# Kernel optimization log

Measured on AMD Instinct MI355X. Metric: run time of the kernel, lower is better.

The kernel has to match this reference:

```python
import jax, jax.numpy as jnp
import numpy as np
from jax import lax

N = 10000
T_CTX = 24
HORIZON = 40
T = T_CTX + HORIZON  # 64
N_ENV = 17
COORD = 2
N_IN = N_ENV + COORD + 2  # 21
H = 128


def _lstm_cell(inp, h, c, Wih, Whh, bih, bhh):
    # torch.nn.LSTMCell gate order: input, forget, cell, output
    g = inp @ Wih.T + bih + h @ Whh.T + bhh  # [N, 4H]
    i, f, gg, o = jnp.split(g, 4, axis=1)
    c2 = jax.nn.sigmoid(f) * c + jax.nn.sigmoid(i) * jnp.tanh(gg)
    h2 = jax.nn.sigmoid(o) * jnp.tanh(c2)
    return h2, c2


def setup_inputs() -> dict:
    key = jax.random.key(0)
    ks = jax.random.split(key, 30)
    kaiming = lambda k, shp: jax.random.normal(k, shp, jnp.float32) * np.sqrt(2.0 / shp[-1]).astype(np.float32)
    u = 1.0 / np.sqrt(H).astype(np.float32)
    uni = lambda k, shp: jax.random.uniform(k, shp, jnp.float32, -u, u)
    inp = {
        'x': jax.random.uniform(ks[0], (N, T), jnp.float32),
        'coords': jax.random.normal(ks[1], (N, COORD), jnp.float32),
        'env': jax.random.normal(ks[2], (N, N_ENV, T), jnp.float32),
        'areas': jax.random.uniform(ks[3], (N,), jnp.float32),
        # encoder params (2 stacked H->H LSTM layers)
        'W_enc_in': kaiming(ks[4], (H, N_IN)),
        'enc_Wih': uni(ks[5], (2, 4 * H, H)),
        'enc_Whh': uni(ks[6], (2, 4 * H, H)),
        'enc_bih': uni(ks[7], (2, 4 * H)),
        'enc_bhh': uni(ks[8], (2, 4 * H)),
        # decoder NodeLSTM params
        'W_dec_in': kaiming(ks[9], (H, N_IN)),
        'in_Wih': uni(ks[10], (4 * H, 2 * H)),  # lstm_in takes [proj, enc_state]
        'in_Whh': uni(ks[11], (4 * H, H)),
        'in_bih': uni(ks[12], (4 * H,)),
        'in_bhh': uni(ks[13], (4 * H,)),
        'd_Wih': uni(ks[14], (4 * H, H)),
        'd_Whh': uni(ks[15], (4 * H, H)),
        'd_bih': uni(ks[16], (4 * H,)),
        'd_bhh': uni(ks[17], (4 * H,)),
        # SourceSinkMLP params
        'mlp_W1': kaiming(ks[18], (H, H + N_IN)),
        'mlp_b1': jnp.zeros((H,), jnp.float32),
        'mlp_W2': kaiming(ks[19], (2, H)),
        'mlp_b2': jnp.zeros((2,), jnp.float32),
    }
    return inp


def reference(x, coords, env, areas, W_enc_in, enc_Wih, enc_Whh, enc_bih, enc_bhh,
              W_dec_in, in_Wih, in_Whh, in_bih, in_bhh, d_Wih, d_Whh, d_bih, d_bhh,
              mlp_W1, mlp_b1, mlp_W2, mlp_b2):
    n = x.shape[0]
    areas_c = areas[:, None]
    x_seq = x.T                              # [T, N]
    env_seq = jnp.transpose(env, (2, 0, 1))  # [T, N, N_ENV]
    z = jnp.zeros((n, H), x.dtype)

    # ---- RecurrentEncoder over context steps ----
    def enc_step(carry, xs):
        h0, c0, h1, c1 = carry
        xt, et = xs
        inp = jnp.concatenate([xt[:, None], coords, et, areas_c], axis=1)  # [N, N_IN]
        proj = inp @ W_enc_in.T
        h0, c0 = _lstm_cell(proj, h0, c0, enc_Wih[0], enc_Whh[0], enc_bih[0], enc_bhh[0])
        h1, c1 = _lstm_cell(h0, h1, c1, enc_Wih[1], enc_Whh[1], enc_bih[1], enc_bhh[1])
        return (h0, c0, h1, c1), None

    (h0, c0, h1, c1), _ = lax.scan(enc_step, (z, z, z, z), (x_seq[:T_CTX], env_seq[:T_CTX]))
    enc_state = h1  # captured once in setup_states, constant over the forecast

    # ---- NodeLSTM + SourceSinkMLP rollout over the horizon ----
    def dec_step(carry, et):
        xc, h0, c0, h1, c1 = carry  # xc: [N, 1]
        inp = jnp.concatenate([xc, coords, et, areas_c], axis=1)  # [N, N_IN]
        proj = jnp.concatenate([inp @ W_dec_in.T, enc_state], axis=1)  # [N, 2H]
        h0, c0 = _lstm_cell(proj, h0, c0, in_Wih, in_Whh, in_bih, in_bhh)
        h1, c1 = _lstm_cell(h0, h1, c1, d_Wih, d_Whh, d_bih, d_bhh)
        # SourceSinkMLP
        zmid = jax.nn.leaky_relu(jnp.concatenate([h1, inp], axis=1) @ mlp_W1.T + mlp_b1)
        ss = zmid @ mlp_W2.T + mlp_b2  # [N, 2]
        source = jax.nn.sigmoid(ss[:, :1])
        sink = jax.nn.sigmoid(ss[:, 1:2]) * xc
        xn = xc + source - sink
        return (xn, h0, c0, h1, c1), xn[:, 0]

    x0 = x[:, T_CTX - 1][:, None]
    _, ys = lax.scan(dec_step, (x0, h0, c0, h1, c1), env_seq[T_CTX:T_CTX + HORIZON])
    return ys.T  # [N, HORIZON]
```

## Files before the change

kernel.cpp:

```cpp
#include <hip/hip_runtime.h>

#define NTOT  10000
#define TALL  64
#define TCTX  24
#define HOR   40
#define HH    128
#define G4    512
#define NENV  17
#define SAMP  16

typedef __attribute__((ext_vector_type(8))) short  bf16x8;
typedef __attribute__((ext_vector_type(4))) float  f32x4;
typedef unsigned short u16;

#define SEG_W0E   0
#define SEG_W0D   8192
#define SEG_WIH1  16384
#define SEG_WHH1  24576
#define SEG_DWIH  32768
#define SEG_DWHH  40960
#define SEG_M0E   49152
#define SEG_MDE   51200
#define SEG_WIHH  53248
#define SEG_W1H   61440
#define SEG_W1I   63488
#define NFRAGS    64000

#define L_MDL   0
#define L_W1H   32768
#define L_W1I   65536
#define L_BASE  73728
#define L_H0    106496
#define L_H1    115200
#define L_ZMS   123904
#define L_INPS  128256
#define L_XBLK  129536
#define L_W2L   131072
#define L_XCS   132096
#define SMEM_TOTAL 132160

__device__ __forceinline__ float sigf(float v)   { return 1.0f/(1.0f + __expf(-v)); }
__device__ __forceinline__ float tanhf_(float v) { return 1.0f - 2.0f/(__expf(2.0f*v) + 1.0f); }
__device__ __forceinline__ u16 f2bf(float f){
    unsigned int u = __float_as_uint(f);
    u += 0x7fffu + ((u >> 16) & 1u);
    return (u16)(u >> 16);
}
__device__ __forceinline__ float bf2f(u16 h){ return __uint_as_float(((unsigned int)h) << 16); }

__global__ void fold_kernel(const float* __restrict__ enc_Wih, const float* __restrict__ enc_Whh,
                            const float* __restrict__ W_enc_in,
                            const float* __restrict__ in_Wih,  const float* __restrict__ in_Whh,
                            const float* __restrict__ W_dec_in,
                            const float* __restrict__ dWih,    const float* __restrict__ dWhh,
                            const float* __restrict__ mlp_W1,  const float* __restrict__ mlp_b1,
                            const float* __restrict__ enc_bih, const float* __restrict__ enc_bhh,
                            const float* __restrict__ in_bih,  const float* __restrict__ in_bhh,
                            void* __restrict__ ws)
{
    int fid = blockIdx.x*256 + threadIdx.x;
    if (fid >= NFRAGS) return;
    const int lane = fid & 63;
    const int cc = lane & 15;
    const int kg = lane >> 4;
    float vals[8];

    if (fid < 49152) {
        int segi = fid >> 13;
        int loc  = fid & 8191;
        int gt   = loc >> 8;
        int kb   = (loc >> 6) & 3;
        int r    = gt*16 + cc;
        int k0   = kb*32 + kg*8;
        const float* src;
        switch (segi) {
            case 0: src = enc_Whh;          break;
            case 1: src = in_Whh;           break;
            case 2: src = enc_Wih + 65536;  break;
            case 3: src = enc_Whh + 65536;  break;
            case 4: src = dWih;             break;
            default: src = dWhh;            break;
        }
        #pragma unroll
        for (int j = 0; j < 8; ++j) vals[j] = src[(size_t)r*128 + k0 + j];
    } else if (fid < 53248) {
        int loc = fid - 49152;
        int which = loc >> 11; loc &= 2047;
        int gt = loc >> 6;
        int r  = gt*16 + cc;
        int k0 = kg*8;
        const float* A = which ? (in_Wih + (size_t)r*256) : (enc_Wih + (size_t)r*128);
        const float* B = which ? W_dec_in : W_enc_in;
        float bias = which ? (in_bih[r] + in_bhh[r]) : (enc_bih[r] + enc_bhh[r]);
        #pragma unroll
        for (int j = 0; j < 8; ++j) {
            int k = k0 + j;
            float v = 0.f;
            int c = (k <= 16) ? (3 + k) : (k == 17 ? 0 : (k == 18 ? 1 : (k == 19 ? 2 : (k == 20 ? 20 : -1))));
            if (k == 21) v = bias;
            else if (c >= 0) {
                float a = 0.f;
                for (int h = 0; h < HH; ++h) a = fmaf(A[h], B[h*21 + c], a);
                v = a;
            }
            vals[j] = v;
        }
    } else if (fid < 61440) {
        int loc = fid - 53248;
        int gt = loc >> 8; int kb = (loc >> 6) & 3;
        int r = gt*16 + cc; int k0 = kb*32 + kg*8;
        #pragma unroll
        for (int j = 0; j < 8; ++j) vals[j] = in_Wih[(size_t)r*256 + 128 + k0 + j];
    } else if (fid < 63488) {
        int loc = fid - 61440;
        int gt = loc >> 8; int kb = (loc >> 6) & 3;
        int r = gt*16 + cc; int k0 = kb*32 + kg*8;
        #pragma unroll
        for (int j = 0; j < 8; ++j) vals[j] = mlp_W1[(size_t)r*149 + k0 + j];
    } else {
        int loc = fid - 63488;
        int gt = loc >> 6;
        int r = gt*16 + cc; int k0 = kg*8;
        #pragma unroll
        for (int j = 0; j < 8; ++j) {
            int k = k0 + j; float v = 0.f;
            if (k <= 16)      v = mlp_W1[(size_t)r*149 + 131 + k];
            else if (k == 17) v = mlp_W1[(size_t)r*149 + 128];
            else if (k == 18) v = mlp_W1[(size_t)r*149 + 129];
            else if (k == 19) v = mlp_W1[(size_t)r*149 + 130];
            else if (k == 20) v = mlp_W1[(size_t)r*149 + 148];
            else if (k == 21) v = mlp_b1[r];
            vals[j] = v;
        }
    }
    union { uint4 u4; u16 us[8]; } pk;
    #pragma unroll
    for (int j = 0; j < 8; ++j) pk.us[j] = f2bf(vals[j]);
    *(uint4*)((char*)ws + (size_t)fid*16) = pk.u4;
}

__global__ __launch_bounds__(512, 1)
void lstm_main(const float* __restrict__ x, const float* __restrict__ coords,
               const float* __restrict__ env, const float* __restrict__ areas,
               const float* __restrict__ enc_bih, const float* __restrict__ enc_bhh,
               const float* __restrict__ dbih,   const float* __restrict__ dbhh,
               const float* __restrict__ mlp_W2, const float* __restrict__ mlp_b2,
               const void* __restrict__ ws, float* __restrict__ out)
{
    extern __shared__ char smem[];
    u16*   MdL  = (u16*)(smem + L_MDL);
    u16*   W1Hl = (u16*)(smem + L_W1H);
    u16*   W1Il = (u16*)(smem + L_W1I);
    float* baseL= (float*)(smem + L_BASE);
    u16*   zms  = (u16*)(smem + L_ZMS);
    u16*   inps = (u16*)(smem + L_INPS);
    float* xblk = (float*)(smem + L_XBLK);
    float* w2l  = (float*)(smem + L_W2L);
    float* xcs  = (float*)(smem + L_XCS);

    const int tid  = threadIdx.x;
    const int lane = tid & 63;
    const int wid  = tid >> 6;
    const int cc   = lane & 15;
    const int kg   = lane >> 4;
    const int s0   = blockIdx.x * SAMP;
    const char* wsb = (const char*)ws;
    const f32x4 zero4 = {0.f, 0.f, 0.f, 0.f};

    #pragma unroll
    for (int i = 0; i < 4; ++i) {
        ((uint4*)(smem + L_MDL))[i*512 + tid] = ((const uint4*)wsb)[SEG_M0E + i*512 + tid];
        ((uint4*)(smem + L_W1H))[i*512 + tid] = ((const uint4*)wsb)[SEG_W1H + i*512 + tid];
    }
    ((uint4*)(smem + L_W1I))[tid] = ((const uint4*)wsb)[SEG_W1I + tid];
    for (int i = tid; i < 2176; i += 512) {
        ((u16*)(smem + L_H0 + 4352))[i] = 0;
        ((u16*)(smem + L_H1 + 4352))[i] = 0;
    }
    if (tid < 384) xblk[tid] = x[(size_t)(s0 + tid/24)*TALL + (tid % 24)];
    if (tid < 256) w2l[tid] = mlp_W2[tid];
    if (tid < SAMP) {
        inps[tid*40 + 18] = f2bf(coords[(size_t)(s0+tid)*2 + 0]);
        inps[tid*40 + 19] = f2bf(coords[(size_t)(s0+tid)*2 + 1]);
        inps[tid*40 + 20] = f2bf(areas[s0+tid]);
        inps[tid*40 + 21] = 0x3F80;
        #pragma unroll
        for (int c = 22; c < 32; ++c) inps[tid*40 + c] = 0;
    }

    const int sA = tid / NENV, eA = tid - sA*NENV;
    const bool envth = (tid < 272);
    const float* envp = env + ((size_t)(s0 + (envth ? sA : 0))*NENV + (envth ? eA : 0))*TALL;
    float evA = envth ? envp[0] : 0.f;

    bf16x8 W0r[16], WrA[16], WrB[16];
    float  lb1[4];
    #pragma unroll
    for (int g = 0; g < 4; ++g) {
        int gt = g*8 + wid;
        #pragma unroll
        for (int kb = 0; kb < 4; ++kb) {
            W0r[g*4+kb] = *(const bf16x8*)(wsb + ((size_t)(SEG_W0E  + (gt*4+kb)*64 + lane))*16);
            WrA[g*4+kb] = *(const bf16x8*)(wsb + ((size_t)(SEG_WIH1 + (gt*4+kb)*64 + lane))*16);
            WrB[g*4+kb] = *(const bf16x8*)(wsb + ((size_t)(SEG_WHH1 + (gt*4+kb)*64 + lane))*16);
        }
        int grow = gt*16 + cc;
        lb1[g] = enc_bih[512 + grow] + enc_bhh[512 + grow];
    }

    float c0r[4] = {0.f,0.f,0.f,0.f};
    float c1r[4] = {0.f,0.f,0.f,0.f};
    __syncthreads();

    #pragma unroll 1
    for (int t = 0; t < TCTX; ++t) {
        u16* h0w = (u16*)(smem + L_H0 + (t&1)*4352);
        u16* h0r = (u16*)(smem + L_H0 + ((t&1)^1)*4352);
        u16* h1w = (u16*)(smem + L_H1 + (t&1)*4352);
        u16* h1r = (u16*)(smem + L_H1 + ((t&1)^1)*4352);

        if (envth)    inps[sA*40 + eA]  = f2bf(evA);
        if (tid < 16) inps[tid*40 + 17] = f2bf(xblk[tid*24 + t]);
        __syncthreads();
        if (envth && t+1 < TALL) evA = envp[t+1];

        bf16x8 ia = *(const bf16x8*)(inps + cc*40 + kg*8);
        f32x4 acc[4];
        #pragma unroll
        for (int g = 0; g < 4; ++g) {
            bf16x8 md = *(const bf16x8*)(MdL + ((size_t)((g*8+wid)*64 + lane))*8);
            acc[g] = __builtin_amdgcn_mfma_f32_16x16x32_bf16(ia, md, zero4, 0, 0, 0);
        }
        #pragma unroll
        for (int kb = 0; kb < 4; ++kb) {
            bf16x8 ha = *(const bf16x8*)(h0r + cc*136 + kb*32 + kg*8);
            #pragma unroll
            for (int g = 0; g < 4; ++g)
                acc[g] = __builtin_amdgcn_mfma_f32_16x16x32_bf16(ha, W0r[g*4+kb], acc[g], 0, 0, 0);
        }
        float h2[4];
        #pragma unroll
        for (int r = 0; r < 4; ++r) {
            float c2 = fmaf(sigf(acc[1][r]), c0r[r], sigf(acc[0][r])*tanhf_(acc[2][r]));
            c0r[r] = c2;
            h2[r] = sigf(acc[3][r])*tanhf_(c2);
        }
        #pragma unroll
        for (int r = 0; r < 4; ++r)
            h0w[(kg*4+r)*136 + wid*16 + cc] = f2bf(h2[r]);
        __syncthreads();

        #pragma unroll
        for (int g = 0; g < 4; ++g) { f32x4 v = {lb1[g],lb1[g],lb1[g],lb1[g]}; acc[g] = v; }
        #pragma unroll
        for (int kb = 0; kb < 4; ++kb) {
            bf16x8 ha = *(const bf16x8*)(h0w + cc*136 + kb*32 + kg*8);
            #pragma unroll
            for (int g = 0; g < 4; ++g)
                acc[g] = __builtin_amdgcn_mfma_f32_16x16x32_bf16(ha, WrA[g*4+kb], acc[g], 0, 0, 0);
        }
        #pragma unroll
        for (int kb = 0; kb < 4; ++kb) {
            bf16x8 ha = *(const bf16x8*)(h1r + cc*136 + kb*32 + kg*8);
            #pragma unroll
            for (int g = 0; g < 4; ++g)
                acc[g] = __builtin_amdgcn_mfma_f32_16x16x32_bf16(ha, WrB[g*4+kb], acc[g], 0, 0, 0);
        }
        #pragma unroll
        for (int r = 0; r < 4; ++r) {
            float c2 = fmaf(sigf(acc[1][r]), c1r[r], sigf(acc[0][r])*tanhf_(acc[2][r]));
            c1r[r] = c2;
            h2[r] = sigf(acc[3][r])*tanhf_(c2);
        }
        #pragma unroll
        for (int r = 0; r < 4; ++r)
            h1w[(kg*4+r)*136 + wid*16 + cc] = f2bf(h2[r]);
    }

    __syncthreads();

    {
        u16* hEnc = (u16*)(smem + L_H1 + 4352);
        f32x4 bD[4];
        #pragma unroll
        for (int g = 0; g < 4; ++g) bD[g] = zero4;
        #pragma unroll
        for (int kb = 0; kb < 4; ++kb) {
            bf16x8 ha = *(const bf16x8*)(hEnc + cc*136 + kb*32 + kg*8);
            #pragma unroll
            for (int g = 0; g < 4; ++g) {
                bf16x8 wb = *(const bf16x8*)(wsb + ((size_t)(SEG_WIHH + ((g*8+wid)*4+kb)*64 + lane))*16);
                bD[g] = __builtin_amdgcn_mfma_f32_16x16x32_bf16(ha, wb, bD[g], 0, 0, 0);
            }
        }
        #pragma unroll
        for (int g = 0; g < 4; ++g)
            *(f32x4*)(baseL + ((size_t)((wid*4+g)*64 + lane))*4) = bD[g];
    }
    #pragma unroll
    for (int g = 0; g < 4; ++g) {
        int gt = g*8 + wid;
        #pragma unroll
        for (int kb = 0; kb < 4; ++kb) {
            W0r[g*4+kb] = *(const bf16x8*)(wsb + ((size_t)(SEG_W0D  + (gt*4+kb)*64 + lane))*16);
            WrA[g*4+kb] = *(const bf16x8*)(wsb + ((size_t)(SEG_DWIH + (gt*4+kb)*64 + lane))*16);
            WrB[g*4+kb] = *(const bf16x8*)(wsb + ((size_t)(SEG_DWHH + (gt*4+kb)*64 + lane))*16);
        }
        int grow = gt*16 + cc;
        lb1[g] = dbih[grow] + dbhh[grow];
    }
    #pragma unroll
    for (int i = 0; i < 4; ++i)
        ((uint4*)(smem + L_MDL))[i*512 + tid] = ((const uint4*)wsb)[SEG_MDE + i*512 + tid];
    if (tid < SAMP) {
        float xv = xblk[tid*24 + 23];
        xcs[tid] = xv;
        inps[tid*40 + 17] = f2bf(xv);
    }
    const float b20 = mlp_b2[0], b21 = mlp_b2[1];
    const int hs = lane >> 2, hq = lane & 3;
    __syncthreads();

    #pragma unroll 1
    for (int td = 0; td < HOR; ++td) {
        const int q = td & 1;
        u16* h0w = (u16*)(smem + L_H0 + q*4352);
        u16* h0r = (u16*)(smem + L_H0 + (q^1)*4352);
        u16* h1w = (u16*)(smem + L_H1 + q*4352);
        u16* h1r = (u16*)(smem + L_H1 + (q^1)*4352);

        if (envth) inps[sA*40 + eA] = f2bf(evA);
        __syncthreads();
        if (envth && TCTX+td+1 < TALL) evA = envp[TCTX+td+1];

        bf16x8 ia = *(const bf16x8*)(inps + cc*40 + kg*8);
        f32x4 acc[4];
        #pragma unroll
        for (int g = 0; g < 4; ++g) {
            f32x4 cb = *(const f32x4*)(baseL + ((size_t)((wid*4+g)*64 + lane))*4);
            bf16x8 md = *(const bf16x8*)(MdL + ((size_t)((g*8+wid)*64 + lane))*8);
            acc[g] = __builtin_amdgcn_mfma_f32_16x16x32_bf16(ia, md, cb, 0, 0, 0);
        }
        #pragma unroll
        for (int kb = 0; kb < 4; ++kb) {
            bf16x8 ha = *(const bf16x8*)(h0r + cc*136 + kb*32 + kg*8);
            #pragma unroll
            for (int g = 0; g < 4; ++g)
                acc[g] = __builtin_amdgcn_mfma_f32_16x16x32_bf16(ha, W0r[g*4+kb], acc[g], 0, 0, 0);
        }
        float h2[4];
        #pragma unroll
        for (int r = 0; r < 4; ++r) {
            float c2 = fmaf(sigf(acc[1][r]), c0r[r], sigf(acc[0][r])*tanhf_(acc[2][r]));
            c0r[r] = c2;
            h2[r] = sigf(acc[3][r])*tanhf_(c2);
        }
        #pragma unroll
        for (int r = 0; r < 4; ++r)
            h0w[(kg*4+r)*136 + wid*16 + cc] = f2bf(h2[r]);
        __syncthreads();

        #pragma unroll
        for (int g = 0; g < 4; ++g) { f32x4 v = {lb1[g],lb1[g],lb1[g],lb1[g]}; acc[g] = v; }
        #pragma unroll
        for (int kb = 0; kb < 4; ++kb) {
            bf16x8 ha = *(const bf16x8*)(h0w + cc*136 + kb*32 + kg*8);
            #pragma unroll
            for (int g = 0; g < 4; ++g)
                acc[g] = __builtin_amdgcn_mfma_f32_16x16x32_bf16(ha, WrA[g*4+kb], acc[g], 0, 0, 0);
        }
        #pragma unroll
        for (int kb = 0; kb < 4; ++kb) {
            bf16x8 ha = *(const bf16x8*)(h1r + cc*136 + kb*32 + kg*8);
            #pragma unroll
            for (int g = 0; g < 4; ++g)
                acc[g] = __builtin_amdgcn_mfma_f32_16x16x32_bf16(ha, WrB[g*4+kb], acc[g], 0, 0, 0);
        }
        #pragma unroll
        for (int r = 0; r < 4; ++r) {
            float c2 = fmaf(sigf(acc[1][r]), c1r[r], sigf(acc[0][r])*tanhf_(acc[2][r]));
            c1r[r] = c2;
            h2[r] = sigf(acc[3][r])*tanhf_(c2);
        }
        #pragma unroll
        for (int r = 0; r < 4; ++r)
            h1w[(kg*4+r)*136 + wid*16 + cc] = f2bf(h2[r]);
        __syncthreads();

        bf16x8 w1i = *(const bf16x8*)(W1Il + ((size_t)(wid*64 + lane))*8);
        f32x4 macc = __builtin_amdgcn_mfma_f32_16x16x32_bf16(ia, w1i, zero4, 0, 0, 0);
        #pragma unroll
        for (int kb = 0; kb < 4; ++kb) {
            bf16x8 ha = *(const bf16x8*)(h1w + cc*136 + kb*32 + kg*8);
            bf16x8 wb = *(const bf16x8*)(W1Hl + ((size_t)((wid*4+kb)*64 + lane))*8);
            macc = __builtin_amdgcn_mfma_f32_16x16x32_bf16(ha, wb, macc, 0, 0, 0);
        }
        #pragma unroll
        for (int r = 0; r < 4; ++r) {
            float z = macc[r];
            z = (z > 0.f) ? z : 0.01f*z;
            zms[(kg*4+r)*136 + wid*16 + cc] = f2bf(z);
        }
        __syncthreads();

        if (wid == 0) {
            float xch = xcs[hs];
            float a0 = 0.f, a1 = 0.f;
            #pragma unroll
            for (int c8 = 0; c8 < 4; ++c8) {
                bf16x8 z8 = *(const bf16x8*)(zms + hs*136 + hq*32 + c8*8);
                #pragma unroll
                for (int j = 0; j < 8; ++j) {
                    float zf = bf2f((u16)z8[j]);
                    int u = hq*32 + c8*8 + j;
                    a0 = fmaf(zf, w2l[u], a0);
                    a1 = fmaf(zf, w2l[128 + u], a1);
                }
            }
            a0 += __shfl_xor(a0, 1); a0 += __shfl_xor(a0, 2);
            a1 += __shfl_xor(a1, 1); a1 += __shfl_xor(a1, 2);
            float xn = xch + sigf(a0 + b20) - sigf(a1 + b21)*xch;
            if (hq == 0) {
                xcs[hs] = xn;
                inps[hs*40 + 17] = f2bf(xn);
                out[(size_t)(s0 + hs)*HOR + td] = xn;
            }
        }
    }
}

extern "C" void kernel_launch(void* const* d_in, const int* in_sizes, int n_in,
                              void* d_out, int out_size, void* d_ws, size_t ws_size,
                              hipStream_t stream)
{
    const float* x        = (const float*)d_in[0];
    const float* coords   = (const float*)d_in[1];
    const float* env      = (const float*)d_in[2];
    const float* areas    = (const float*)d_in[3];
    const float* W_enc_in = (const float*)d_in[4];
    const float* enc_Wih  = (const float*)d_in[5];
    const float* enc_Whh  = (const float*)d_in[6];
    const float* enc_bih  = (const float*)d_in[7];
    const float* enc_bhh  = (const float*)d_in[8];
    const float* W_dec_in = (const float*)d_in[9];
    const float* in_Wih   = (const float*)d_in[10];
    const float* in_Whh   = (const float*)d_in[11];
    const float* in_bih   = (const float*)d_in[12];
    const float* in_bhh   = (const float*)d_in[13];
    const float* dWih     = (const float*)d_in[14];
    const float* dWhh     = (const float*)d_in[15];
    const float* dbih     = (const float*)d_in[16];
    const float* dbhh     = (const float*)d_in[17];
    const float* mlp_W1   = (const float*)d_in[18];
    const float* mlp_b1   = (const float*)d_in[19];
    const float* mlp_W2   = (const float*)d_in[20];
    const float* mlp_b2   = (const float*)d_in[21];
    float* out = (float*)d_out;

    fold_kernel<<<dim3(250), dim3(256), 0, stream>>>(
        enc_Wih, enc_Whh, W_enc_in, in_Wih, in_Whh, W_dec_in,
        dWih, dWhh, mlp_W1, mlp_b1, enc_bih, enc_bhh, in_bih, in_bhh, d_ws);

    hipFuncSetAttribute((const void*)lstm_main,
                        hipFuncAttributeMaxDynamicSharedMemorySize, SMEM_TOTAL);
    lstm_main<<<dim3(NTOT/SAMP), dim3(512), SMEM_TOTAL, stream>>>(
        x, coords, env, areas, enc_bih, enc_bhh, dbih, dbhh, mlp_W2, mlp_b2, d_ws, out);
    (void)in_sizes; (void)n_in; (void)out_size; (void)ws_size;
}
```

Measured before the change: 1.010 ms.

## Process 32 samples per block reusing register-resident weights across two M-tiles

Doubles samples per workgroup from 16 to 32. Each wave now issues two MFMA row tiles against the same register-held weight fragments, so weight reuse per load doubles and the grid shrinks from 625 to 313 blocks. The decoder base term moves to bf16 in LDS, layer-1 biases move to LDS, and an extra barrier is added before the h0 write to protect the buffer. Tail samples are clamped and guarded. Risks include more register pressure from the doubled accumulators and cell state, a waves_per_eu hint, and the rounding of the base term to bf16.

```diff
diff --git a/kernel.cpp b/kernel.cpp
--- a/kernel.cpp
+++ b/kernel.cpp
@@ -5,13 +5,14 @@
 #define TCTX  24
 #define HOR   40
 #define HH    128
-#define G4    512
 #define NENV  17
-#define SAMP  16
+#define SAMP  32
+#define NB    313
 
 typedef __attribute__((ext_vector_type(8))) short  bf16x8;
 typedef __attribute__((ext_vector_type(4))) float  f32x4;
 typedef unsigned short u16;
+typedef unsigned int   u32;
 
 #define SEG_W0E   0
 #define SEG_W0D   8192
@@ -31,22 +32,26 @@
 #define L_W1I   65536
 #define L_BASE  73728
 #define L_H0    106496
-#define L_H1    115200
-#define L_ZMS   123904
-#define L_INPS  128256
-#define L_XBLK  129536
-#define L_W2L   131072
-#define L_XCS   132096
-#define SMEM_TOTAL 132160
+#define L_H1    123904
+#define L_ZMS   141312
+#define L_INPS  150016
+#define L_XBLK  152576
+#define L_W2L   155648
+#define L_XCS   156672
+#define L_LB1   156800
+#define SMEM_TOTAL 158848
+#define HSTR  136
+#define HBUF  8704
 
 __device__ __forceinline__ float sigf(float v)   { return 1.0f/(1.0f + __expf(-v)); }
 __device__ __forceinline__ float tanhf_(float v) { return 1.0f - 2.0f/(__expf(2.0f*v) + 1.0f); }
 __device__ __forceinline__ u16 f2bf(float f){
-    unsigned int u = __float_as_uint(f);
+    u32 u = __float_as_uint(f);
     u += 0x7fffu + ((u >> 16) & 1u);
     return (u16)(u >> 16);
 }
-__device__ __forceinline__ float bf2f(u16 h){ return __uint_as_float(((unsigned int)h) << 16); }
+__device__ __forceinline__ float bf2f(u16 h){ return __uint_as_float(((u32)h) << 16); }
+__device__ __forceinline__ int mini(int a, int b){ return a < b ? a : b; }
 
 __global__ void fold_kernel(const float* __restrict__ enc_Wih, const float* __restrict__ enc_Whh,
                             const float* __restrict__ W_enc_in,
@@ -139,24 +144,25 @@
     *(uint4*)((char*)ws + (size_t)fid*16) = pk.u4;
 }
 
-__global__ __launch_bounds__(512, 1)
-void lstm_main(const float* __restrict__ x, const float* __restrict__ coords,
-               const float* __restrict__ env, const float* __restrict__ areas,
-               const float* __restrict__ enc_bih, const float* __restrict__ enc_bhh,
-               const float* __restrict__ dbih,   const float* __restrict__ dbhh,
-               const float* __restrict__ mlp_W2, const float* __restrict__ mlp_b2,
-               const void* __restrict__ ws, float* __restrict__ out)
+__global__ void __launch_bounds__(512)
+__attribute__((amdgpu_waves_per_eu(2)))
+lstm_main(const float* __restrict__ x, const float* __restrict__ coords,
+          const float* __restrict__ env, const float* __restrict__ areas,
+          const float* __restrict__ enc_bih, const float* __restrict__ enc_bhh,
+          const float* __restrict__ dbih,   const float* __restrict__ dbhh,
+          const float* __restrict__ mlp_W2, const float* __restrict__ mlp_b2,
+          const void* __restrict__ ws, float* __restrict__ out)
 {
     extern __shared__ char smem[];
     u16*   MdL  = (u16*)(smem + L_MDL);
-    u16*   W1Hl = (u16*)(smem + L_W1H);
     u16*   W1Il = (u16*)(smem + L_W1I);
-    float* baseL= (float*)(smem + L_BASE);
+    u16*   baseL= (u16*)(smem + L_BASE);
     u16*   zms  = (u16*)(smem + L_ZMS);
     u16*   inps = (u16*)(smem + L_INPS);
     float* xblk = (float*)(smem + L_XBLK);
     float* w2l  = (float*)(smem + L_W2L);
     float* xcs  = (float*)(smem + L_XCS);
+    float* lb1L = (float*)(smem + L_LB1);
 
     const int tid  = threadIdx.x;
     const int lane = tid & 63;
@@ -165,36 +171,45 @@
     const int kg   = lane >> 4;
     const int s0   = blockIdx.x * SAMP;
     const char* wsb = (const char*)ws;
+    const uint4* w4 = (const uint4*)ws;
     const f32x4 zero4 = {0.f, 0.f, 0.f, 0.f};
 
     #pragma unroll
     for (int i = 0; i < 4; ++i) {
-        ((uint4*)(smem + L_MDL))[i*512 + tid] = ((const uint4*)wsb)[SEG_M0E + i*512 + tid];
-        ((uint4*)(smem + L_W1H))[i*512 + tid] = ((const uint4*)wsb)[SEG_W1H + i*512 + tid];
-    }
-    ((uint4*)(smem + L_W1I))[tid] = ((const uint4*)wsb)[SEG_W1I + tid];
-    for (int i = tid; i < 2176; i += 512) {
-        ((u16*)(smem + L_H0 + 4352))[i] = 0;
-        ((u16*)(smem + L_H1 + 4352))[i] = 0;
-    }
-    if (tid < 384) xblk[tid] = x[(size_t)(s0 + tid/24)*TALL + (tid % 24)];
+        ((uint4*)(smem + L_MDL))[i*512 + tid] = w4[SEG_M0E + i*512 + tid];
+        ((uint4*)(smem + L_W1H))[i*512 + tid] = w4[SEG_W1H + i*512 + tid];
+    }
+    ((uint4*)(smem + L_W1I))[tid] = w4[SEG_W1I + tid];
+    for (int i = tid; i < 4352; i += 512) {
+        ((u16*)(smem + L_H0 + HBUF))[i] = 0;
+        ((u16*)(smem + L_H1 + HBUF))[i] = 0;
+    }
+    for (int i = tid; i < SAMP*TCTX; i += 512) {
+        int sc = mini(s0 + i/TCTX, NTOT-1);
+        xblk[i] = x[(size_t)sc*TALL + (i % TCTX)];
+    }
     if (tid < 256) w2l[tid] = mlp_W2[tid];
+    lb1L[tid] = enc_bih[512 + tid] + enc_bhh[512 + tid];
     if (tid < SAMP) {
-        inps[tid*40 + 18] = f2bf(coords[(size_t)(s0+tid)*2 + 0]);
-        inps[tid*40 + 19] = f2bf(coords[(size_t)(s0+tid)*2 + 1]);
-        inps[tid*40 + 20] = f2bf(areas[s0+tid]);
+        int sc = mini(s0 + tid, NTOT-1);
+        inps[tid*40 + 18] = f2bf(coords[(size_t)sc*2 + 0]);
+        inps[tid*40 + 19] = f2bf(coords[(size_t)sc*2 + 1]);
+        inps[tid*40 + 20] = f2bf(areas[sc]);
         inps[tid*40 + 21] = 0x3F80;
         #pragma unroll
         for (int c = 22; c < 32; ++c) inps[tid*40 + c] = 0;
     }
 
     const int sA = tid / NENV, eA = tid - sA*NENV;
-    const bool envth = (tid < 272);
-    const float* envp = env + ((size_t)(s0 + (envth ? sA : 0))*NENV + (envth ? eA : 0))*TALL;
-    float evA = envth ? envp[0] : 0.f;
+    const int iB = tid + 512;
+    const int sB = iB / NENV, eB = iB - sB*NENV;
+    const float* envpA = env + ((size_t)mini(s0 + sA, NTOT-1)*NENV + eA)*TALL;
+    const float* envpB = env + ((size_t)mini(s0 + ((tid < 32) ? sB : 0), NTOT-1)*NENV
+                                + ((tid < 32) ? eB : 0))*TALL;
+    float evA = envpA[0];
+    float evB = (tid < 32) ? envpB[0] : 0.f;
 
     bf16x8 W0r[16], WrA[16], WrB[16];
-    float  lb1[4];
     #pragma unroll
     for (int g = 0; g < 4; ++g) {
         int gt = g*8 + wid;
@@ -204,98 +219,131 @@
             WrA[g*4+kb] = *(const bf16x8*)(wsb + ((size_t)(SEG_WIH1 + (gt*4+kb)*64 + lane))*16);
             WrB[g*4+kb] = *(const bf16x8*)(wsb + ((size_t)(SEG_WHH1 + (gt*4+kb)*64 + lane))*16);
         }
-        int grow = gt*16 + cc;
-        lb1[g] = enc_bih[512 + grow] + enc_bhh[512 + grow];
-    }
-
-    float c0r[4] = {0.f,0.f,0.f,0.f};
-    float c1r[4] = {0.f,0.f,0.f,0.f};
+    }
+
+    float c0r[8], c1r[8];
+    #pragma unroll
+    for (int i = 0; i < 8; ++i) { c0r[i] = 0.f; c1r[i] = 0.f; }
     __syncthreads();
 
     #pragma unroll 1
     for (int t = 0; t < TCTX; ++t) {
-        u16* h0w = (u16*)(smem + L_H0 + (t&1)*4352);
-        u16* h0r = (u16*)(smem + L_H0 + ((t&1)^1)*4352);
-        u16* h1w = (u16*)(smem + L_H1 + (t&1)*4352);
-        u16* h1r = (u16*)(smem + L_H1 + ((t&1)^1)*4352);
-
-        if (envth)    inps[sA*40 + eA]  = f2bf(evA);
-        if (tid < 16) inps[tid*40 + 17] = f2bf(xblk[tid*24 + t]);
-        __syncthreads();
-        if (envth && t+1 < TALL) evA = envp[t+1];
-
-        bf16x8 ia = *(const bf16x8*)(inps + cc*40 + kg*8);
-        f32x4 acc[4];
+        u16* h0w = (u16*)(smem + L_H0 + (t&1)*HBUF);
+        u16* h0r = (u16*)(smem + L_H0 + ((t&1)^1)*HBUF);
+        u16* h1w = (u16*)(smem + L_H1 + (t&1)*HBUF);
+        u16* h1r = (u16*)(smem + L_H1 + ((t&1)^1)*HBUF);
+
+        inps[sA*40 + eA] = f2bf(evA);
+        if (tid < 32) { inps[sB*40 + eB] = f2bf(evB); inps[tid*40 + 17] = f2bf(xblk[tid*TCTX + t]); }
+        __syncthreads();
+        evA = envpA[t+1];
+        if (tid < 32) evB = envpB[t+1];
+
+        bf16x8 ia0 = *(const bf16x8*)(inps + cc*40 + kg*8);
+        bf16x8 ia1 = *(const bf16x8*)(inps + (16+cc)*40 + kg*8);
+        f32x4 acc[8];
         #pragma unroll
         for (int g = 0; g < 4; ++g) {
             bf16x8 md = *(const bf16x8*)(MdL + ((size_t)((g*8+wid)*64 + lane))*8);
-            acc[g] = __builtin_amdgcn_mfma_f32_16x16x32_bf16(ia, md, zero4, 0, 0, 0);
-        }
-        #pragma unroll
-        for (int kb = 0; kb < 4; ++kb) {
-            bf16x8 ha = *(const bf16x8*)(h0r + cc*136 + kb*32 + kg*8);
-            #pragma unroll
-            for (int g = 0; g < 4; ++g)
-                acc[g] = __builtin_amdgcn_mfma_f32_16x16x32_bf16(ha, W0r[g*4+kb], acc[g], 0, 0, 0);
-        }
-        float h2[4];
+            acc[0+g] = __builtin_amdgcn_mfma_f32_16x16x32_bf16(ia0, md, zero4, 0, 0, 0);
+            acc[4+g] = __builtin_amdgcn_mfma_f32_16x16x32_bf16(ia1, md, zero4, 0, 0, 0);
+        }
+        #pragma unroll
+        for (int kb = 0; kb < 4; ++kb) {
+            bf16x8 ha0 = *(const bf16x8*)(h0r + cc*HSTR + kb*32 + kg*8);
+            bf16x8 ha1 = *(const bf16x8*)(h0r + (16+cc)*HSTR + kb*32 + kg*8);
+            #pragma unroll
+            for (int g = 0; g < 4; ++g) {
+                acc[0+g] = __builtin_amdgcn_mfma_f32_16x16x32_bf16(ha0, W0r[g*4+kb], acc[0+g], 0, 0, 0);
+                acc[4+g] = __builtin_amdgcn_mfma_f32_16x16x32_bf16(ha1, W0r[g*4+kb], acc[4+g], 0, 0, 0);
+            }
+        }
+        float h2[8];
+        #pragma unroll
+        for (int ts = 0; ts < 2; ++ts)
         #pragma unroll
         for (int r = 0; r < 4; ++r) {
-            float c2 = fmaf(sigf(acc[1][r]), c0r[r], sigf(acc[0][r])*tanhf_(acc[2][r]));
-            c0r[r] = c2;
-            h2[r] = sigf(acc[3][r])*tanhf_(c2);
-        }
+            float c2 = fmaf(sigf(acc[ts*4+1][r]), c0r[ts*4+r], sigf(acc[ts*4+0][r])*tanhf_(acc[ts*4+2][r]));
+            c0r[ts*4+r] = c2;
+            h2[ts*4+r] = sigf(acc[ts*4+3][r])*tanhf_(c2);
+        }
+        __syncthreads();
+        #pragma unroll
+        for (int ts = 0; ts < 2; ++ts)
         #pragma unroll
         for (int r = 0; r < 4; ++r)
-            h0w[(kg*4+r)*136 + wid*16 + cc] = f2bf(h2[r]);
-        __syncthreads();
-
-        #pragma unroll
-        for (int g = 0; g < 4; ++g) { f32x4 v = {lb1[g],lb1[g],lb1[g],lb1[g]}; acc[g] = v; }
-        #pragma unroll
-        for (int kb = 0; kb < 4; ++kb) {
-            bf16x8 ha = *(const bf16x8*)(h0w + cc*136 + kb*32 + kg*8);
-            #pragma unroll
-            for (int g = 0; g < 4; ++g)
-                acc[g] = __builtin_amdgcn_mfma_f32_16x16x32_bf16(ha, WrA[g*4+kb], acc[g], 0, 0, 0);
-        }
-        #pragma unroll
-        for (int kb = 0; kb < 4; ++kb) {
-            bf16x8 ha = *(const bf16x8*)(h1r + cc*136 + kb*32 + kg*8);
-            #pragma unroll
-            for (int g = 0; g < 4; ++g)
-                acc[g] = __builtin_amdgcn_mfma_f32_16x16x32_bf16(ha, WrB[g*4+kb], acc[g], 0, 0, 0);
-        }
+            h0w[(ts*16 + kg*4 + r)*HSTR + wid*16 + cc] = f2bf(h2[ts*4+r]);
+        __syncthreads();
+
+        {
+            float b0 = lb1L[(0*8+wid)*16 + cc], b1g = lb1L[(1*8+wid)*16 + cc];
+            float b2g = lb1L[(2*8+wid)*16 + cc], b3 = lb1L[(3*8+wid)*16 + cc];
+            f32x4 v0 = {b0,b0,b0,b0}, v1 = {b1g,b1g,b1g,b1g}, v2 = {b2g,b2g,b2g,b2g}, v3 = {b3,b3,b3,b3};
+            acc[0]=v0; acc[1]=v1; acc[2]=v2; acc[3]=v3;
+            acc[4]=v0; acc[5]=v1; acc[6]=v2; acc[7]=v3;
+        }
+        #pragma unroll
+        for (int kb = 0; kb < 4; ++kb) {
+            bf16x8 ha0 = *(const bf16x8*)(h0w + cc*HSTR + kb*32 + kg*8);
+            bf16x8 ha1 = *(const bf16x8*)(h0w + (16+cc)*HSTR + kb*32 + kg*8);
+            #pragma unroll
+            for (int g = 0; g < 4; ++g) {
+                acc[0+g] = __builtin_amdgcn_mfma_f32_16x16x32_bf16(ha0, WrA[g*4+kb], acc[0+g], 0, 0, 0);
+                acc[4+g] = __builtin_amdgcn_mfma_f32_16x16x32_bf16(ha1, WrA[g*4+kb], acc[4+g], 0, 0, 0);
+            }
+        }
+        #pragma unroll
+        for (int kb = 0; kb < 4; ++kb) {
+            bf16x8 ha0 = *(const bf16x8*)(h1r + cc*HSTR + kb*32 + kg*8);
+            bf16x8 ha1 = *(const bf16x8*)(h1r + (16+cc)*HSTR + kb*32 + kg*8);
+            #pragma unroll
+            for (int g = 0; g < 4; ++g) {
+                acc[0+g] = __builtin_amdgcn_mfma_f32_16x16x32_bf16(ha0, WrB[g*4+kb], acc[0+g], 0, 0, 0);
+                acc[4+g] = __builtin_amdgcn_mfma_f32_16x16x32_bf16(ha1, WrB[g*4+kb], acc[4+g], 0, 0, 0);
+            }
+        }
+        #pragma unroll
+        for (int ts = 0; ts < 2; ++ts)
         #pragma unroll
         for (int r = 0; r < 4; ++r) {
-            float c2 = fmaf(sigf(acc[1][r]), c1r[r], sigf(acc[0][r])*tanhf_(acc[2][r]));
-            c1r[r] = c2;
-            h2[r] = sigf(acc[3][r])*tanhf_(c2);
-        }
+            float c2 = fmaf(sigf(acc[ts*4+1][r]), c1r[ts*4+r], sigf(acc[ts*4+0][r])*tanhf_(acc[ts*4+2][r]));
+            c1r[ts*4+r] = c2;
+            h2[ts*4+r] = sigf(acc[ts*4+3][r])*tanhf_(c2);
+        }
+        #pragma unroll
+        for (int ts = 0; ts < 2; ++ts)
         #pragma unroll
         for (int r = 0; r < 4; ++r)
-            h1w[(kg*4+r)*136 + wid*16 + cc] = f2bf(h2[r]);
+            h1w[(ts*16 + kg*4 + r)*HSTR + wid*16 + cc] = f2bf(h2[ts*4+r]);
     }
 
     __syncthreads();
 
     {
-        u16* hEnc = (u16*)(smem + L_H1 + 4352);
-        f32x4 bD[4];
-        #pragma unroll
-        for (int g = 0; g < 4; ++g) bD[g] = zero4;
-        #pragma unroll
-        for (int kb = 0; kb < 4; ++kb) {
-            bf16x8 ha = *(const bf16x8*)(hEnc + cc*136 + kb*32 + kg*8);
+        u16* hEnc = (u16*)(smem + L_H1 + HBUF);
+        f32x4 bD[8];
+        #pragma unroll
+        for (int i = 0; i < 8; ++i) bD[i] = zero4;
+        #pragma unroll
+        for (int kb = 0; kb < 4; ++kb) {
+            bf16x8 ha0 = *(const bf16x8*)(hEnc + cc*HSTR + kb*32 + kg*8);
+            bf16x8 ha1 = *(const bf16x8*)(hEnc + (16+cc)*HSTR + kb*32 + kg*8);
             #pragma unroll
             for (int g = 0; g < 4; ++g) {
                 bf16x8 wb = *(const bf16x8*)(wsb + ((size_t)(SEG_WIHH + ((g*8+wid)*4+kb)*64 + lane))*16);
-                bD[g] = __builtin_amdgcn_mfma_f32_16x16x32_bf16(ha, wb, bD[g], 0, 0, 0);
-            }
-        }
-        #pragma unroll
-        for (int g = 0; g < 4; ++g)
-            *(f32x4*)(baseL + ((size_t)((wid*4+g)*64 + lane))*4) = bD[g];
+                bD[0+g] = __builtin_amdgcn_mfma_f32_16x16x32_bf16(ha0, wb, bD[0+g], 0, 0, 0);
+                bD[4+g] = __builtin_amdgcn_mfma_f32_16x16x32_bf16(ha1, wb, bD[4+g], 0, 0, 0);
+            }
+        }
+        #pragma unroll
+        for (int ts = 0; ts < 2; ++ts)
+        #pragma unroll
+        for (int g = 0; g < 4; ++g) {
+            union { uint2 u2; u16 us[4]; } pk;
+            #pragma unroll
+            for (int r = 0; r < 4; ++r) pk.us[r] = f2bf(bD[ts*4+g][r]);
+            *(uint2*)(baseL + ts*8192 + ((wid*4+g)*64 + lane)*4) = pk.u2;
+        }
     }
     #pragma unroll
     for (int g = 0; g < 4; ++g) {
@@ -306,14 +354,13 @@
             WrA[g*4+kb] = *(const bf16x8*)(wsb + ((size_t)(SEG_DWIH + (gt*4+kb)*64 + lane))*16);
             WrB[g*4+kb] = *(const bf16x8*)(wsb + ((size_t)(SEG_DWHH + (gt*4+kb)*64 + lane))*16);
         }
-        int grow = gt*16 + cc;
-        lb1[g] = dbih[grow] + dbhh[grow];
     }
     #pragma unroll
     for (int i = 0; i < 4; ++i)
-        ((uint4*)(smem + L_MDL))[i*512 + tid] = ((const uint4*)wsb)[SEG_MDE + i*512 + tid];
+        ((uint4*)(smem + L_MDL))[i*512 + tid] = w4[SEG_MDE + i*512 + tid];
+    lb1L[tid] = dbih[tid] + dbhh[tid];
     if (tid < SAMP) {
-        float xv = xblk[tid*24 + 23];
+        float xv = xblk[tid*TCTX + (TCTX-1)];
         xcs[tid] = xv;
         inps[tid*40 + 17] = f2bf(xv);
     }
@@ -324,91 +371,127 @@
     #pragma unroll 1
     for (int td = 0; td < HOR; ++td) {
         const int q = td & 1;
-        u16* h0w = (u16*)(smem + L_H0 + q*4352);
-        u16* h0r = (u16*)(smem + L_H0 + (q^1)*4352);
-        u16* h1w = (u16*)(smem + L_H1 + q*4352);
-        u16* h1r = (u16*)(smem + L_H1 + (q^1)*4352);
-
-        if (envth) inps[sA*40 + eA] = f2bf(evA);
-        __syncthreads();
-        if (envth && TCTX+td+1 < TALL) evA = envp[TCTX+td+1];
-
-        bf16x8 ia = *(const bf16x8*)(inps + cc*40 + kg*8);
-        f32x4 acc[4];
+        const int t = TCTX + td;
+        u16* h0w = (u16*)(smem + L_H0 + q*HBUF);
+        u16* h0r = (u16*)(smem + L_H0 + (q^1)*HBUF);
+        u16* h1w = (u16*)(smem + L_H1 + q*HBUF);
+        u16* h1r = (u16*)(smem + L_H1 + (q^1)*HBUF);
+
+        inps[sA*40 + eA] = f2bf(evA);
+        if (tid < 32) inps[sB*40 + eB] = f2bf(evB);
+        __syncthreads();
+        if (t + 1 < TALL) { evA = envpA[t+1]; if (tid < 32) evB = envpB[t+1]; }
+
+        bf16x8 ia0 = *(const bf16x8*)(inps + cc*40 + kg*8);
+        bf16x8 ia1 = *(const bf16x8*)(inps + (16+cc)*40 + kg*8);
+        f32x4 acc[8];
+        #pragma unroll
+        for (int ts = 0; ts < 2; ++ts)
         #pragma unroll
         for (int g = 0; g < 4; ++g) {
-            f32x4 cb = *(const f32x4*)(baseL + ((size_t)((wid*4+g)*64 + lane))*4);
+            union { uint2 u2; u16 us[4]; } pk;
+            pk.u2 = *(const uint2*)(baseL + ts*8192 + ((wid*4+g)*64 + lane)*4);
+            f32x4 cb = { bf2f(pk.us[0]), bf2f(pk.us[1]), bf2f(pk.us[2]), bf2f(pk.us[3]) };
             bf16x8 md = *(const bf16x8*)(MdL + ((size_t)((g*8+wid)*64 + lane))*8);
-            acc[g] = __builtin_amdgcn_mfma_f32_16x16x32_bf16(ia, md, cb, 0, 0, 0);
-        }
-        #pragma unroll
-        for (int kb = 0; kb < 4; ++kb) {
-            bf16x8 ha = *(const bf16x8*)(h0r + cc*136 + kb*32 + kg*8);
-            #pragma unroll
-            for (int g = 0; g < 4; ++g)
-                acc[g] = __builtin_amdgcn_mfma_f32_16x16x32_bf16(ha, W0r[g*4+kb], acc[g], 0, 0, 0);
-        }
-        float h2[4];
+            acc[ts*4+g] = __builtin_amdgcn_mfma_f32_16x16x32_bf16(ts ? ia1 : ia0, md, cb, 0, 0, 0);
+        }
+        #pragma unroll
+        for (int kb = 0; kb < 4; ++kb) {
+            bf16x8 ha0 = *(const bf16x8*)(h0r + cc*HSTR + kb*32 + kg*8);
+            bf16x8 ha1 = *(const bf16x8*)(h0r + (16+cc)*HSTR + kb*32 + kg*8);
+            #pragma unroll
+            for (int g = 0; g < 4; ++g) {
+                acc[0+g] = __builtin_amdgcn_mfma_f32_16x16x32_bf16(ha0, W0r[g*4+kb], acc[0+g], 0, 0, 0);
+                acc[4+g] = __builtin_amdgcn_mfma_f32_16x16x32_bf16(ha1, W0r[g*4+kb], acc[4+g], 0, 0, 0);
+            }
+        }
+        float h2[8];
+        #pragma unroll
+        for (int ts = 0; ts < 2; ++ts)
         #pragma unroll
         for (int r = 0; r < 4; ++r) {
-            float c2 = fmaf(sigf(acc[1][r]), c0r[r], sigf(acc[0][r])*tanhf_(acc[2][r]));
-            c0r[r] = c2;
-            h2[r] = sigf(acc[3][r])*tanhf_(c2);
-        }
+            float c2 = fmaf(sigf(acc[ts*4+1][r]), c0r[ts*4+r], sigf(acc[ts*4+0][r])*tanhf_(acc[ts*4+2][r]));
+            c0r[ts*4+r] = c2;
+            h2[ts*4+r] = sigf(acc[ts*4+3][r])*tanhf_(c2);
+        }
+        __syncthreads();
+        #pragma unroll
+        for (int ts = 0; ts < 2; ++ts)
         #pragma unroll
         for (int r = 0; r < 4; ++r)
-            h0w[(kg*4+r)*136 + wid*16 + cc] = f2bf(h2[r]);
-        __syncthreads();
-
-        #pragma unroll
-        for (int g = 0; g < 4; ++g) { f32x4 v = {lb1[g],lb1[g],lb1[g],lb1[g]}; acc[g] = v; }
-        #pragma unroll
-        for (int kb = 0; kb < 4; ++kb) {
-            bf16x8 ha = *(const bf16x8*)(h0w + cc*136 + kb*32 + kg*8);
-            #pragma unroll
-            for (int g = 0; g < 4; ++g)
-                acc[g] = __builtin_amdgcn_mfma_f32_16x16x32_bf16(ha, WrA[g*4+kb], acc[g], 0, 0, 0);
-        }
-        #pragma unroll
-        for (int kb = 0; kb < 4; ++kb) {
-            bf16x8 ha = *(const bf16x8*)(h1r + cc*136 + kb*32 + kg*8);
-            #pragma unroll
-            for (int g = 0; g < 4; ++g)
-                acc[g] = __builtin_amdgcn_mfma_f32_16x16x32_bf16(ha, WrB[g*4+kb], acc[g], 0, 0, 0);
-        }
+            h0w[(ts*16 + kg*4 + r)*HSTR + wid*16 + cc] = f2bf(h2[ts*4+r]);
+        __syncthreads();
+
+        {
+            float b0 = lb1L[(0*8+wid)*16 + cc], b1g = lb1L[(1*8+wid)*16 + cc];
+            float b2g = lb1L[(2*8+wid)*16 + cc], b3 = lb1L[(3*8+wid)*16 + cc];
+            f32x4 v0 = {b0,b0,b0,b0}, v1 = {b1g,b1g,b1g,b1g}, v2 = {b2g,b2g,b2g,b2g}, v3 = {b3,b3,b3,b3};
+            acc[0]=v0; acc[1]=v1; acc[2]=v2; acc[3]=v3;
+            acc[4]=v0; acc[5]=v1; acc[6]=v2; acc[7]=v3;
+        }
+        #pragma unroll
+        for (int kb = 0; kb < 4; ++kb) {
+            bf16x8 ha0 = *(const bf16x8*)(h0w + cc*HSTR + kb*32 + kg*8);
+            bf16x8 ha1 = *(const bf16x8*)(h0w + (16+cc)*HSTR + kb*32 + kg*8);
+            #pragma unroll
+            for (int g = 0; g < 4; ++g) {
+                acc[0+g] = __builtin_amdgcn_mfma_f32_16x16x32_bf16(ha0, WrA[g*4+kb], acc[0+g], 0, 0, 0);
+                acc[4+g] = __builtin_amdgcn_mfma_f32_16x16x32_bf16(ha1, WrA[g*4+kb], acc[4+g], 0, 0, 0);
+            }
+        }
+        #pragma unroll
+        for (int kb = 0; kb < 4; ++kb) {
+            bf16x8 ha0 = *(const bf16x8*)(h1r + cc*HSTR + kb*32 + kg*8);
+            bf16x8 ha1 = *(const bf16x8*)(h1r + (16+cc)*HSTR + kb*32 + kg*8);
+            #pragma unroll
+            for (int g = 0; g < 4; ++g) {
+                acc[0+g] = __builtin_amdgcn_mfma_f32_16x16x32_bf16(ha0, WrB[g*4+kb], acc[0+g], 0, 0, 0);
+                acc[4+g] = __builtin_amdgcn_mfma_f32_16x16x32_bf16(ha1, WrB[g*4+kb], acc[4+g], 0, 0, 0);
+            }
+        }
+        #pragma unroll
+        for (int ts = 0; ts < 2; ++ts)
         #pragma unroll
         for (int r = 0; r < 4; ++r) {
-            float c2 = fmaf(sigf(acc[1][r]), c1r[r], sigf(acc[0][r])*tanhf_(acc[2][r]));
-            c1r[r] = c2;
-            h2[r] = sigf(acc[3][r])*tanhf_(c2);
-        }
+            float c2 = fmaf(sigf(acc[ts*4+1][r]), c1r[ts*4+r], sigf(acc[ts*4+0][r])*tanhf_(acc[ts*4+2][r]));
+            c1r[ts*4+r] = c2;
+            h2[ts*4+r] = sigf(acc[ts*4+3][r])*tanhf_(c2);
+        }
+        #pragma unroll
+        for (int ts = 0; ts < 2; ++ts)
         #pragma unroll
         for (int r = 0; r < 4; ++r)
-            h1w[(kg*4+r)*136 + wid*16 + cc] = f2bf(h2[r]);
+            h1w[(ts*16 + kg*4 + r)*HSTR + wid*16 + cc] = f2bf(h2[ts*4+r]);
         __syncthreads();
 
         bf16x8 w1i = *(const bf16x8*)(W1Il + ((size_t)(wid*64 + lane))*8);
-        f32x4 macc = __builtin_amdgcn_mfma_f32_16x16x32_bf16(ia, w1i, zero4, 0, 0, 0);
-        #pragma unroll
-        for (int kb = 0; kb < 4; ++kb) {
-            bf16x8 ha = *(const bf16x8*)(h1w + cc*136 + kb*32 + kg*8);
-            bf16x8 wb = *(const bf16x8*)(W1Hl + ((size_t)((wid*4+kb)*64 + lane))*8);
-            macc = __builtin_amdgcn_mfma_f32_16x16x32_bf16(ha, wb, macc, 0, 0, 0);
+        f32x4 m0 = __builtin_amdgcn_mfma_f32_16x16x32_bf16(ia0, w1i, zero4, 0, 0, 0);
+        f32x4 m1 = __builtin_amdgcn_mfma_f32_16x16x32_bf16(ia1, w1i, zero4, 0, 0, 0);
+        #pragma unroll
+        for (int kb = 0; kb < 4; ++kb) {
+            bf16x8 ha0 = *(const bf16x8*)(h1w + cc*HSTR + kb*32 + kg*8);
+            bf16x8 ha1 = *(const bf16x8*)(h1w + (16+cc)*HSTR + kb*32 + kg*8);
+            bf16x8 wb = *(const bf16x8*)((u16*)(smem + L_W1H) + ((size_t)((wid*4+kb)*64 + lane))*8);
+            m0 = __builtin_amdgcn_mfma_f32_16x16x32_bf16(ha0, wb, m0, 0, 0, 0);
+            m1 = __builtin_amdgcn_mfma_f32_16x16x32_bf16(ha1, wb, m1, 0, 0, 0);
         }
         #pragma unroll
         for (int r = 0; r < 4; ++r) {
-            float z = macc[r];
-            z = (z > 0.f) ? z : 0.01f*z;
-            zms[(kg*4+r)*136 + wid*16 + cc] = f2bf(z);
-        }
-        __syncthreads();
-
-        if (wid == 0) {
-            float xch = xcs[hs];
+            float z0 = m0[r]; z0 = (z0 > 0.f) ? z0 : 0.01f*z0;
+            float z1 = m1[r]; z1 = (z1 > 0.f) ? z1 : 0.01f*z1;
+            zms[(kg*4 + r)*HSTR + wid*16 + cc] = f2bf(z0);
+            zms[(16 + kg*4 + r)*HSTR + wid*16 + cc] = f2bf(z1);
+        }
+        __syncthreads();
+
+        if (wid < 2) {
+            const int sidx = wid*16 + hs;
+            float xch = xcs[sidx];
+            const u16* zr = zms + sidx*HSTR;
             float a0 = 0.f, a1 = 0.f;
             #pragma unroll
             for (int c8 = 0; c8 < 4; ++c8) {
-                bf16x8 z8 = *(const bf16x8*)(zms + hs*136 + hq*32 + c8*8);
+                bf16x8 z8 = *(const bf16x8*)(zr + hq*32 + c8*8);
                 #pragma unroll
                 for (int j = 0; j < 8; ++j) {
                     float zf = bf2f((u16)z8[j]);
@@ -421,9 +504,9 @@
             a1 += __shfl_xor(a1, 1); a1 += __shfl_xor(a1, 2);
             float xn = xch + sigf(a0 + b20) - sigf(a1 + b21)*xch;
             if (hq == 0) {
-                xcs[hs] = xn;
-                inps[hs*40 + 17] = f2bf(xn);
-                out[(size_t)(s0 + hs)*HOR + td] = xn;
+                xcs[sidx] = xn;
+                inps[sidx*40 + 17] = f2bf(xn);
+                if (s0 + sidx < NTOT) out[(size_t)(s0 + sidx)*HOR + td] = xn;
             }
         }
     }
@@ -463,7 +546,7 @@
 
     hipFuncSetAttribute((const void*)lstm_main,
                         hipFuncAttributeMaxDynamicSharedMemorySize, SMEM_TOTAL);
-    lstm_main<<<dim3(NTOT/SAMP), dim3(512), SMEM_TOTAL, stream>>>(
+    lstm_main<<<dim3(NB), dim3(512), SMEM_TOTAL, stream>>>(
         x, coords, env, areas, enc_bih, enc_bhh, dbih, dbhh, mlp_W2, mlp_b2, d_ws, out);
     (void)in_sizes; (void)n_in; (void)out_size; (void)ws_size;
 }
```

Result: slower. 1.556 ms (+54.1%).

## Stream recurrent LSTM weights from global memory instead of holding them in registers

Applied to the files above, without the earlier changes.

Drops the register-resident Wih/Whh fragment arrays for the second LSTM layer in both the encoder and decoder. Those fragments are now loaded from the workspace inside each timestep's MFMA loop, and the kernel is relaxed to target two waves per EU. The aim is to cut VGPR pressure so more waves can be resident to hide latency. In exchange, every step issues extra global or L2 loads on the recurrent critical path, and LDS usage may still cap occupancy at one block per CU.

```diff
diff --git a/kernel.cpp b/kernel.cpp
--- a/kernel.cpp
+++ b/kernel.cpp
@@ -12,6 +12,7 @@
 typedef __attribute__((ext_vector_type(8))) short  bf16x8;
 typedef __attribute__((ext_vector_type(4))) float  f32x4;
 typedef unsigned short u16;
+typedef unsigned int   u32;
 
 #define SEG_W0E   0
 #define SEG_W0D   8192
@@ -42,11 +43,11 @@
 __device__ __forceinline__ float sigf(float v)   { return 1.0f/(1.0f + __expf(-v)); }
 __device__ __forceinline__ float tanhf_(float v) { return 1.0f - 2.0f/(__expf(2.0f*v) + 1.0f); }
 __device__ __forceinline__ u16 f2bf(float f){
-    unsigned int u = __float_as_uint(f);
+    u32 u = __float_as_uint(f);
     u += 0x7fffu + ((u >> 16) & 1u);
     return (u16)(u >> 16);
 }
-__device__ __forceinline__ float bf2f(u16 h){ return __uint_as_float(((unsigned int)h) << 16); }
+__device__ __forceinline__ float bf2f(u16 h){ return __uint_as_float(((u32)h) << 16); }
 
 __global__ void fold_kernel(const float* __restrict__ enc_Wih, const float* __restrict__ enc_Whh,
                             const float* __restrict__ W_enc_in,
@@ -139,13 +140,14 @@
     *(uint4*)((char*)ws + (size_t)fid*16) = pk.u4;
 }
 
-__global__ __launch_bounds__(512, 1)
-void lstm_main(const float* __restrict__ x, const float* __restrict__ coords,
-               const float* __restrict__ env, const float* __restrict__ areas,
-               const float* __restrict__ enc_bih, const float* __restrict__ enc_bhh,
-               const float* __restrict__ dbih,   const float* __restrict__ dbhh,
-               const float* __restrict__ mlp_W2, const float* __restrict__ mlp_b2,
-               const void* __restrict__ ws, float* __restrict__ out)
+__global__ void __launch_bounds__(512)
+__attribute__((amdgpu_waves_per_eu(2)))
+lstm_main(const float* __restrict__ x, const float* __restrict__ coords,
+          const float* __restrict__ env, const float* __restrict__ areas,
+          const float* __restrict__ enc_bih, const float* __restrict__ enc_bhh,
+          const float* __restrict__ dbih,   const float* __restrict__ dbhh,
+          const float* __restrict__ mlp_W2, const float* __restrict__ mlp_b2,
+          const void* __restrict__ ws, float* __restrict__ out)
 {
     extern __shared__ char smem[];
     u16*   MdL  = (u16*)(smem + L_MDL);
@@ -193,17 +195,14 @@
     const float* envp = env + ((size_t)(s0 + (envth ? sA : 0))*NENV + (envth ? eA : 0))*TALL;
     float evA = envth ? envp[0] : 0.f;
 
-    bf16x8 W0r[16], WrA[16], WrB[16];
+    bf16x8 W0r[16];
     float  lb1[4];
     #pragma unroll
     for (int g = 0; g < 4; ++g) {
         int gt = g*8 + wid;
         #pragma unroll
-        for (int kb = 0; kb < 4; ++kb) {
-            W0r[g*4+kb] = *(const bf16x8*)(wsb + ((size_t)(SEG_W0E  + (gt*4+kb)*64 + lane))*16);
-            WrA[g*4+kb] = *(const bf16x8*)(wsb + ((size_t)(SEG_WIH1 + (gt*4+kb)*64 + lane))*16);
-            WrB[g*4+kb] = *(const bf16x8*)(wsb + ((size_t)(SEG_WHH1 + (gt*4+kb)*64 + lane))*16);
-        }
+        for (int kb = 0; kb < 4; ++kb)
+            W0r[g*4+kb] = *(const bf16x8*)(wsb + ((size_t)(SEG_W0E + (gt*4+kb)*64 + lane))*16);
         int grow = gt*16 + cc;
         lb1[g] = enc_bih[512 + grow] + enc_bhh[512 + grow];
     }
@@ -256,15 +255,19 @@
         for (int kb = 0; kb < 4; ++kb) {
             bf16x8 ha = *(const bf16x8*)(h0w + cc*136 + kb*32 + kg*8);
             #pragma unroll
-            for (int g = 0; g < 4; ++g)
-                acc[g] = __builtin_amdgcn_mfma_f32_16x16x32_bf16(ha, WrA[g*4+kb], acc[g], 0, 0, 0);
+            for (int g = 0; g < 4; ++g) {
+                bf16x8 wb = *(const bf16x8*)(wsb + ((size_t)(SEG_WIH1 + ((g*8+wid)*4+kb)*64 + lane))*16);
+                acc[g] = __builtin_amdgcn_mfma_f32_16x16x32_bf16(ha, wb, acc[g], 0, 0, 0);
+            }
         }
         #pragma unroll
         for (int kb = 0; kb < 4; ++kb) {
             bf16x8 ha = *(const bf16x8*)(h1r + cc*136 + kb*32 + kg*8);
             #pragma unroll
-            for (int g = 0; g < 4; ++g)
-                acc[g] = __builtin_amdgcn_mfma_f32_16x16x32_bf16(ha, WrB[g*4+kb], acc[g], 0, 0, 0);
+            for (int g = 0; g < 4; ++g) {
+                bf16x8 wb = *(const bf16x8*)(wsb + ((size_t)(SEG_WHH1 + ((g*8+wid)*4+kb)*64 + lane))*16);
+                acc[g] = __builtin_amdgcn_mfma_f32_16x16x32_bf16(ha, wb, acc[g], 0, 0, 0);
+            }
         }
         #pragma unroll
         for (int r = 0; r < 4; ++r) {
@@ -301,11 +304,8 @@
     for (int g = 0; g < 4; ++g) {
         int gt = g*8 + wid;
         #pragma unroll
-        for (int kb = 0; kb < 4; ++kb) {
-            W0r[g*4+kb] = *(const bf16x8*)(wsb + ((size_t)(SEG_W0D  + (gt*4+kb)*64 + lane))*16);
-            WrA[g*4+kb] = *(const bf16x8*)(wsb + ((size_t)(SEG_DWIH + (gt*4+kb)*64 + lane))*16);
-            WrB[g*4+kb] = *(const bf16x8*)(wsb + ((size_t)(SEG_DWHH + (gt*4+kb)*64 + lane))*16);
-        }
+        for (int kb = 0; kb < 4; ++kb)
+            W0r[g*4+kb] = *(const bf16x8*)(wsb + ((size_t)(SEG_W0D + (gt*4+kb)*64 + lane))*16);
         int grow = gt*16 + cc;
         lb1[g] = dbih[grow] + dbhh[grow];
     }
@@ -366,15 +366,19 @@
         for (int kb = 0; kb < 4; ++kb) {
             bf16x8 ha = *(const bf16x8*)(h0w + cc*136 + kb*32 + kg*8);
             #pragma unroll
-            for (int g = 0; g < 4; ++g)
-                acc[g] = __builtin_amdgcn_mfma_f32_16x16x32_bf16(ha, WrA[g*4+kb], acc[g], 0, 0, 0);
+            for (int g = 0; g < 4; ++g) {
+                bf16x8 wb = *(const bf16x8*)(wsb + ((size_t)(SEG_DWIH + ((g*8+wid)*4+kb)*64 + lane))*16);
+                acc[g] = __builtin_amdgcn_mfma_f32_16x16x32_bf16(ha, wb, acc[g], 0, 0, 0);
+            }
         }
         #pragma unroll
         for (int kb = 0; kb < 4; ++kb) {
             bf16x8 ha = *(const bf16x8*)(h1r + cc*136 + kb*32 + kg*8);
             #pragma unroll
-            for (int g = 0; g < 4; ++g)
-                acc[g] = __builtin_amdgcn_mfma_f32_16x16x32_bf16(ha, WrB[g*4+kb], acc[g], 0, 0, 0);
+            for (int g = 0; g < 4; ++g) {
+                bf16x8 wb = *(const bf16x8*)(wsb + ((size_t)(SEG_DWHH + ((g*8+wid)*4+kb)*64 + lane))*16);
+                acc[g] = __builtin_amdgcn_mfma_f32_16x16x32_bf16(ha, wb, acc[g], 0, 0, 0);
+            }
         }
         #pragma unroll
         for (int r = 0; r < 4; ++r) {
```

Measured after the change: 1.054 ms. 4.3% more time.
